# Performance work log

Measured on AMD Instinct MI355X. Metric: run time of the kernel, lower is better.

## Reference

```python
import jax, jax.numpy as jnp
import numpy as np

B, S, E, H = 2, 2048, 1024, 16
D = E // H  # head_dim = 64


def _rope(x):
    # x: (B, H, S, D); torchtune-style interleaved rotary embedding
    s, d = x.shape[-2], x.shape[-1]
    inv_freq = 1.0 / (10000.0 ** (jnp.arange(0, d, 2, dtype=jnp.float32) / d))  # (d/2,)
    freqs = jnp.arange(s, dtype=jnp.float32)[:, None] * inv_freq[None, :]       # (S, d/2)
    cos, sin = jnp.cos(freqs), jnp.sin(freqs)
    x1, x2 = x[..., 0::2], x[..., 1::2]
    o1 = x1 * cos - x2 * sin
    o2 = x2 * cos + x1 * sin
    return jnp.stack([o1, o2], axis=-1).reshape(x.shape)


def setup_inputs() -> dict:
    key = jax.random.key(0)
    kx, kq, kk, kv, ko = jax.random.split(key, 5)
    std = 1.0 / np.sqrt(E)
    return {
        "x": jax.random.normal(kx, (B, S, E), dtype=jnp.float32),
        "W_q": jax.random.normal(kq, (E, E), dtype=jnp.float32) * std,
        "W_k": jax.random.normal(kk, (E, E), dtype=jnp.float32) * std,
        "W_v": jax.random.normal(kv, (E, E), dtype=jnp.float32) * std,
        "W_o": jax.random.normal(ko, (E, E), dtype=jnp.float32) * std,
    }


def reference(x, W_q, W_k, W_v, W_o):
    b, s, e = x.shape
    h, d = H, e // H
    # nn.Linear: y = x @ W.T  (weights are (out, in))
    q = (x @ W_q.T).reshape(b, s, h, d).transpose(0, 2, 1, 3)  # (B,H,S,D)
    k = (x @ W_k.T).reshape(b, s, h, d).transpose(0, 2, 1, 3)
    v = (x @ W_v.T).reshape(b, s, h, d).transpose(0, 2, 1, 3)
    q = _rope(q)
    k = _rope(k)
    attn_scale = 1.0 / np.sqrt(e)  # NOTE: scales by sqrt(hidden_dim), as in source
    scores = jnp.einsum("bhsd,bhtd->bhst", q, k) * attn_scale  # (B,H,S,S)
    causal = jnp.triu(jnp.ones((s, s), dtype=bool), k=1)
    scores = jnp.where(causal, -jnp.inf, scores)
    probs = jax.nn.softmax(scores, axis=-1)  # dropout is identity in eval
    out = jnp.einsum("bhst,bhtd->bhsd", probs, v)
    out = out.transpose(0, 2, 1, 3).reshape(b, s, e)
    return out @ W_o.T
```

## Files before the change

### kernel.cpp

```cpp
#include <hip/hip_runtime.h>
#include <hip/hip_bf16.h>

#define BATCH 2
#define SEQ   2048
#define EMB   1024
#define NH    16
#define HD    64
#define MROWS (BATCH*SEQ)
#define NX    (MROWS*EMB)
#define NW    (EMB*EMB)

using f32x4  = __attribute__((ext_vector_type(4))) float;
using bf16x8 = __attribute__((ext_vector_type(8))) short;

#define GLOBAL_AS(p) ((const __attribute__((address_space(1))) void*)(p))
#define LDS_AS(p)    ((__attribute__((address_space(3))) void*)(p))

#define ROPE_L2 0.4152410118609203f
#define QSCALE  0.045084220027780106f

__global__ void fused_cast_kernel(const float* __restrict__ x,
                                  const float* __restrict__ Wq,
                                  const float* __restrict__ Wk,
                                  const float* __restrict__ Wv,
                                  const float* __restrict__ Wo,
                                  __hip_bfloat16* __restrict__ xb,
                                  __hip_bfloat16* __restrict__ Wqkvb,
                                  __hip_bfloat16* __restrict__ Wob,
                                  float2* __restrict__ ctab) {
    if (blockIdx.x >= 4096) {
        int e  = (blockIdx.x - 4096) * 256 + threadIdx.x;
        int s  = e >> 5;
        int ip = e & 31;
        float inv = exp2f(-(float)ip * ROPE_L2);
        float fr  = (float)s * inv;
        float2 cs;
        cs.x = cosf(fr);
        cs.y = sinf(fr);
        ctab[e] = cs;
        return;
    }
    size_t i8 = (size_t)(blockIdx.x * 256 + threadIdx.x) * 8;
    const float* src;
    __hip_bfloat16* dst;
    if (i8 < (size_t)NX) {
        src = x + i8;
        dst = xb + i8;
    } else {
        size_t w = i8 - NX;
        int which = (int)(w >> 20);
        size_t local = w & (NW - 1);
        if (which < 3) {
            src = (which == 0 ? Wq : (which == 1 ? Wk : Wv)) + local;
            dst = Wqkvb + w;
        } else {
            src = Wo + local;
            dst = Wob + local;
        }
    }
    float4 a = *(const float4*)(src);
    float4 b = *(const float4*)(src + 4);
    union { uint4 u; ushort s[8]; } o;
    const float* f = (const float*)&a;
#pragma unroll
    for (int j = 0; j < 4; ++j) {
        __hip_bfloat16 h = __float2bfloat16(f[j]);
        o.s[j] = *(ushort*)&h;
    }
    f = (const float*)&b;
#pragma unroll
    for (int j = 0; j < 4; ++j) {
        __hip_bfloat16 h = __float2bfloat16(f[j]);
        o.s[4 + j] = *(ushort*)&h;
    }
    *(uint4*)dst = o.u;
}

__global__ __launch_bounds__(256) void gemm_qkv_kernel(
        const __hip_bfloat16* __restrict__ A,
        const __hip_bfloat16* __restrict__ W,
        __hip_bfloat16* __restrict__ Qo,
        __hip_bfloat16* __restrict__ Ko,
        __hip_bfloat16* __restrict__ Vo,
        const float2* __restrict__ ctab, int M, int K) {
    __shared__ __hip_bfloat16 As[128 * 64];
    __shared__ __hip_bfloat16 Bs[128 * 64];

    const int tid  = threadIdx.x;
    const int wave = tid >> 6;
    const int lane = tid & 63;
    const int quad = lane >> 4;
    const int l16  = lane & 15;
    const int m0   = blockIdx.y * 128;
    const int n0   = blockIdx.x * 128;
    const int wm   = (wave >> 1) * 64;
    const int wn   = (wave & 1) * 64;
    const int xr   = l16 & 7;

    f32x4 acc[4][4] = {};

    for (int k0 = 0; k0 < K; k0 += 64) {
#pragma unroll
        for (int it = 0; it < 4; ++it) {
            int flat = (wave * 4 + it) * 64 + lane;
            int row  = flat >> 3;
            int g    = (flat & 7) ^ (row & 7);
            const __hip_bfloat16* ga = A + (size_t)(m0 + row) * K + k0 + g * 8;
            const __hip_bfloat16* gb = W + (size_t)(n0 + row) * K + k0 + g * 8;
            __builtin_amdgcn_global_load_lds(GLOBAL_AS(ga),
                LDS_AS(As + (size_t)(wave * 4 + it) * 512), 16, 0, 0);
            __builtin_amdgcn_global_load_lds(GLOBAL_AS(gb),
                LDS_AS(Bs + (size_t)(wave * 4 + it) * 512), 16, 0, 0);
        }
        __syncthreads();

#pragma unroll
        for (int kk = 0; kk < 2; ++kk) {
            const int kg = (kk * 4 + quad) ^ xr;
            bf16x8 af[4], bfr[4];
#pragma unroll
            for (int i = 0; i < 4; ++i) {
                af[i]  = *(const bf16x8*)(&As[(wm + i * 16 + l16) * 64 + kg * 8]);
                bfr[i] = *(const bf16x8*)(&Bs[(wn + i * 16 + l16) * 64 + kg * 8]);
            }
#pragma unroll
            for (int i = 0; i < 4; ++i)
#pragma unroll
                for (int j = 0; j < 4; ++j)
                    acc[i][j] = __builtin_amdgcn_mfma_f32_16x16x32_bf16(
                        af[i], bfr[j], acc[i][j], 0, 0, 0);
        }
        __syncthreads();
    }

    const int tens = n0 >> 10;
    __hip_bfloat16* outp = (tens == 0) ? Qo : ((tens == 1) ? Ko : Vo);
    const int nbase = n0 & 1023;
    if (tens < 2) {
        const float sgn   = (l16 & 1) ? 1.0f : -1.0f;
        const float qmul  = (tens == 0) ? QSCALE : 1.0f;
#pragma unroll
        for (int i = 0; i < 4; ++i)
#pragma unroll
            for (int j = 0; j < 4; ++j) {
                int col  = nbase + wn + j * 16 + l16;
                int ip   = ((wn + j * 16 + l16) & 63) >> 1;
                int row0 = m0 + wm + i * 16 + quad * 4;
#pragma unroll
                for (int rr = 0; rr < 4; ++rr) {
                    float v = acc[i][j][rr];
                    float p = __shfl_xor(v, 1);
                    int sp  = (row0 + rr) & (SEQ - 1);
                    float2 cs = ctab[sp * 32 + ip];
                    float o = (v * cs.x + sgn * p * cs.y) * qmul;
                    outp[(size_t)(row0 + rr) * EMB + col] = __float2bfloat16(o);
                }
            }
    } else {
#pragma unroll
        for (int i = 0; i < 4; ++i)
#pragma unroll
            for (int j = 0; j < 4; ++j) {
                int col  = nbase + wn + j * 16 + l16;
                int row0 = m0 + wm + i * 16 + quad * 4;
#pragma unroll
                for (int rr = 0; rr < 4; ++rr)
                    outp[(size_t)(row0 + rr) * EMB + col] = __float2bfloat16(acc[i][j][rr]);
            }
    }
}

__global__ __launch_bounds__(256) void gemm_oproj_kernel(
        const __hip_bfloat16* __restrict__ A,
        const __hip_bfloat16* __restrict__ Bm,
        float* __restrict__ C, int M, int N, int K) {
    __shared__ __hip_bfloat16 As[128 * 64];
    __shared__ __hip_bfloat16 Bs[64 * 64];

    const int tid  = threadIdx.x;
    const int wave = tid >> 6;
    const int lane = tid & 63;
    const int quad = lane >> 4;
    const int l16  = lane & 15;
    const int m0   = blockIdx.y * 128;
    const int n0   = blockIdx.x * 64;
    const int wm   = (wave >> 1) * 64;
    const int wn   = (wave & 1) * 32;
    const int xr   = l16 & 7;

    f32x4 acc[4][2] = {};

    for (int k0 = 0; k0 < K; k0 += 64) {
#pragma unroll
        for (int it = 0; it < 4; ++it) {
            int flat = (wave * 4 + it) * 64 + lane;
            int row  = flat >> 3;
            int g    = (flat & 7) ^ (row & 7);
            const __hip_bfloat16* ga = A + (size_t)(m0 + row) * K + k0 + g * 8;
            __builtin_amdgcn_global_load_lds(GLOBAL_AS(ga),
                LDS_AS(As + (size_t)(wave * 4 + it) * 512), 16, 0, 0);
        }
#pragma unroll
        for (int it = 0; it < 2; ++it) {
            int flat = (wave * 2 + it) * 64 + lane;
            int row  = flat >> 3;
            int g    = (flat & 7) ^ (row & 7);
            const __hip_bfloat16* gb = Bm + (size_t)(n0 + row) * K + k0 + g * 8;
            __builtin_amdgcn_global_load_lds(GLOBAL_AS(gb),
                LDS_AS(Bs + (size_t)(wave * 2 + it) * 512), 16, 0, 0);
        }
        __syncthreads();

#pragma unroll
        for (int kk = 0; kk < 2; ++kk) {
            const int kg = (kk * 4 + quad) ^ xr;
            bf16x8 af[4], bfr[2];
#pragma unroll
            for (int i = 0; i < 4; ++i)
                af[i] = *(const bf16x8*)(&As[(wm + i * 16 + l16) * 64 + kg * 8]);
#pragma unroll
            for (int j = 0; j < 2; ++j)
                bfr[j] = *(const bf16x8*)(&Bs[(wn + j * 16 + l16) * 64 + kg * 8]);
#pragma unroll
            for (int i = 0; i < 4; ++i)
#pragma unroll
                for (int j = 0; j < 2; ++j)
                    acc[i][j] = __builtin_amdgcn_mfma_f32_16x16x32_bf16(
                        af[i], bfr[j], acc[i][j], 0, 0, 0);
        }
        __syncthreads();
    }

#pragma unroll
    for (int i = 0; i < 4; ++i)
#pragma unroll
        for (int j = 0; j < 2; ++j) {
            int col  = n0 + wn + j * 16 + l16;
            int row0 = m0 + wm + i * 16 + quad * 4;
#pragma unroll
            for (int rr = 0; rr < 4; ++rr)
                C[(size_t)(row0 + rr) * N + col] = acc[i][j][rr];
        }
}

__device__ inline uint cvt_pk_bf16(float lo, float hi) {
    uint r;
    asm("v_cvt_pk_bf16_f32 %0, %1, %2" : "=v"(r) : "v"(lo), "v"(hi));
    return r;
}
__device__ inline float exp2_raw(float x) {
    float r;
    asm("v_exp_f32 %0, %1" : "=v"(r) : "v"(x));
    return r;
}

__global__ __launch_bounds__(256) void attn_mfma_kernel(
        const __hip_bfloat16* __restrict__ Qb,
        const __hip_bfloat16* __restrict__ Kb,
        const __hip_bfloat16* __restrict__ Vb,
        __hip_bfloat16* __restrict__ Attnb,
        __hip_bfloat16* __restrict__ Opart,
        float* __restrict__ Lpart) {
    const int bx   = blockIdx.x;
    const int bh   = blockIdx.y;
    const int b    = bh >> 4;
    const int h    = bh & (NH - 1);
    const int tid  = threadIdx.x;
    const int wave = tid >> 6;
    const int lane = tid & 63;
    const int quad = lane >> 4;
    const int l16  = lane & 15;

    __shared__ __hip_bfloat16 Ks[2][64 * 64];
    __shared__ uint VTs[2][64][33];

    const int vtp = tid >> 3;
    const int sg  = tid & 7;
    const int lr  = lane >> 3;
    const int lg  = (lane & 7) ^ lr;
    const size_t ksrc_lane = (size_t)lr * EMB + lg * 8;

    const __hip_bfloat16* Kbase = Kb + (size_t)b * SEQ * EMB + h * HD;
    const __hip_bfloat16* Vbase = Vb + (size_t)b * SEQ * EMB + h * HD;

    union { uint u[4]; bf16x8 v; } onesu;
    onesu.u[0] = 0x3F803F80u; onesu.u[1] = 0x3F803F80u;
    onesu.u[2] = 0x3F803F80u; onesu.u[3] = 0x3F803F80u;
    const bf16x8 ones = onesu.v;

    const bool isA = (bx < 16);
    const int p   = isA ? bx : bx - 16;
    const int q0  = 31 - p;
    const int k00 = isA ? 0 : 17;
    const int n0s = isA ? 17 : (15 - p);
    const int q1  = p;
    const int n1s = isA ? 0 : (p + 1);

    for (int s = 0; s < 2; ++s) {
        const int qt = s ? q1 : q0;
        const int k0 = s ? 0 : k00;
        const int nt = s ? n1s : n0s;
        if (nt <= 0) continue;
        const bool finalSeg = (!isA && s == 1);
        const int wrow = qt * 64 + wave * 16;

        __syncthreads();

        bf16x8 qf[2];
        {
            const __hip_bfloat16* qp =
                Qb + (size_t)(b * SEQ + wrow + l16) * EMB + h * HD + quad * 8;
            qf[0] = *(const bf16x8*)(qp);
            qf[1] = *(const bf16x8*)(qp + 32);
        }

        f32x4 of[4]  = {};
        f32x4 of_sum = {};

        const __hip_bfloat16* kgp = Kbase + (size_t)k0 * 64 * EMB;
        const __hip_bfloat16* vgp = Vbase + (size_t)(k0 * 64 + 2 * vtp) * EMB + sg * 8;
        uint4 vr0 = *(const uint4*)(vgp);
        uint4 vr1 = *(const uint4*)(vgp + EMB);
#pragma unroll
        for (int it = 0; it < 2; ++it)
            __builtin_amdgcn_global_load_lds(
                GLOBAL_AS(kgp + (size_t)(wave * 2 + it) * 8 * EMB + ksrc_lane),
                LDS_AS(&Ks[0][(wave * 2 + it) * 512]), 16, 0, 0);

        for (int i = 0; i < nt; ++i) {
            const int cur = i & 1;
            const int kt  = k0 + i;

            {
                const uint* v0u = (const uint*)&vr0;
                const uint* v1u = (const uint*)&vr1;
#pragma unroll
                for (int j = 0; j < 4; ++j) {
                    VTs[cur][sg * 8 + 2 * j][vtp] =
                        __builtin_amdgcn_perm(v1u[j], v0u[j], 0x05040100u);
                    VTs[cur][sg * 8 + 2 * j + 1][vtp] =
                        __builtin_amdgcn_perm(v1u[j], v0u[j], 0x07060302u);
                }
            }
            __syncthreads();

            if (i + 1 < nt) {
                kgp += (size_t)64 * EMB;
                vgp += (size_t)64 * EMB;
                vr0 = *(const uint4*)(vgp);
                vr1 = *(const uint4*)(vgp + EMB);
#pragma unroll
                for (int it = 0; it < 2; ++it)
                    __builtin_amdgcn_global_load_lds(
                        GLOBAL_AS(kgp + (size_t)(wave * 2 + it) * 8 * EMB + ksrc_lane),
                        LDS_AS(&Ks[cur ^ 1][(wave * 2 + it) * 512]), 16, 0, 0);
            }

            const bool diag = (kt == qt);
            const __hip_bfloat16* KsC = Ks[cur];
            f32x4 sc[4];
            __builtin_amdgcn_s_setprio(1);
#pragma unroll
            for (int mb = 0; mb < 4; ++mb) {
                f32x4 a = {};
                if (!(diag && mb > wave)) {
                    int krow = mb * 16 + l16;
#pragma unroll
                    for (int kb = 0; kb < 2; ++kb) {
                        int kg = (kb * 4 + quad) ^ (krow & 7);
                        bf16x8 kf = *(const bf16x8*)(&KsC[krow * 64 + kg * 8]);
                        a = __builtin_amdgcn_mfma_f32_16x16x32_bf16(kf, qf[kb], a, 0, 0, 0);
                    }
                }
                sc[mb] = a;
            }
            __builtin_amdgcn_s_setprio(0);

            if (diag) {
#pragma unroll
                for (int mb = 0; mb < 4; ++mb)
#pragma unroll
                    for (int r = 0; r < 4; ++r)
                        if (mb * 16 + quad * 4 + r > wave * 16 + l16)
                            sc[mb][r] = -16384.0f;
            }

#pragma unroll
            for (int mb = 0; mb < 4; ++mb)
#pragma unroll
                for (int r = 0; r < 4; ++r)
                    sc[mb][r] = exp2_raw(sc[mb][r]);

            bf16x8 pf[2];
            {
                union { uint u[4]; bf16x8 v; } t;
                t.u[0] = cvt_pk_bf16(sc[0][0], sc[0][1]);
                t.u[1] = cvt_pk_bf16(sc[0][2], sc[0][3]);
                t.u[2] = cvt_pk_bf16(sc[1][0], sc[1][1]);
                t.u[3] = cvt_pk_bf16(sc[1][2], sc[1][3]);
                pf[0] = t.v;
                t.u[0] = cvt_pk_bf16(sc[2][0], sc[2][1]);
                t.u[1] = cvt_pk_bf16(sc[2][2], sc[2][3]);
                t.u[2] = cvt_pk_bf16(sc[3][0], sc[3][1]);
                t.u[3] = cvt_pk_bf16(sc[3][2], sc[3][3]);
                pf[1] = t.v;
            }

            const uint* VT0 = &VTs[cur][0][0];
            __builtin_amdgcn_s_setprio(1);
#pragma unroll
            for (int nb = 0; nb < 4; ++nb) {
                const uint* vrow = VT0 + (size_t)(nb * 16 + l16) * 33;
#pragma unroll
                for (int c = 0; c < 2; ++c) {
                    union { uint u[4]; bf16x8 v; } vf;
                    vf.u[0] = vrow[c * 16 + 2 * quad];
                    vf.u[1] = vrow[c * 16 + 2 * quad + 1];
                    vf.u[2] = vrow[c * 16 + 8 + 2 * quad];
                    vf.u[3] = vrow[c * 16 + 8 + 2 * quad + 1];
                    of[nb] = __builtin_amdgcn_mfma_f32_16x16x32_bf16(
                        pf[c], vf.v, of[nb], 0, 0, 0);
                }
            }
            of_sum = __builtin_amdgcn_mfma_f32_16x16x32_bf16(pf[0], ones, of_sum, 0, 0, 0);
            of_sum = __builtin_amdgcn_mfma_f32_16x16x32_bf16(pf[1], ones, of_sum, 0, 0, 0);
            __builtin_amdgcn_s_setprio(0);
        }

        const int rl0 = quad * 4;
        if (finalSeg) {
            float linv[4];
#pragma unroll
            for (int r = 0; r < 4; ++r)
                linv[r] = 1.0f / of_sum[r];
#pragma unroll
            for (int nb = 0; nb < 4; ++nb)
#pragma unroll
                for (int r = 0; r < 4; ++r) {
                    float v = of[nb][r] * linv[r];
                    Attnb[(size_t)(b * SEQ + wrow + rl0 + r) * EMB + h * HD + nb * 16 + l16] =
                        __float2bfloat16(v);
                }
        } else {
            const int slot = isA ? 0 : 1;
            const size_t lbase = ((size_t)slot * 32 + bh) * SEQ + wrow;
            if (l16 == 0) {
#pragma unroll
                for (int r = 0; r < 4; ++r)
                    Lpart[lbase + rl0 + r] = of_sum[r];
            }
#pragma unroll
            for (int nb = 0; nb < 4; ++nb)
#pragma unroll
                for (int r = 0; r < 4; ++r)
                    Opart[(lbase + rl0 + r) * HD + nb * 16 + l16] =
                        __float2bfloat16(of[nb][r]);
        }
    }
}

__global__ void combine_kernel(const __hip_bfloat16* __restrict__ Opart,
                               const float* __restrict__ Lpart,
                               __hip_bfloat16* __restrict__ Attnb) {
    int idx = blockIdx.x * 256 + threadIdx.x;
    int d8 = idx & 7;
    int s  = 1024 + ((idx >> 3) & 1023);
    int bh = idx >> 13;
    int b  = bh >> 4;
    int h  = bh & (NH - 1);
    int qt = s >> 6;

    size_t base0 = ((size_t)bh * SEQ + s) * HD + d8 * 8;
    bf16x8 o0 = *(const bf16x8*)(Opart + base0);
    float l = Lpart[(size_t)bh * SEQ + s];
    float acc[8];
#pragma unroll
    for (int j = 0; j < 8; ++j)
        acc[j] = __uint_as_float(((uint)(ushort)o0[j]) << 16);
    if (qt >= 17) {
        size_t base1 = ((size_t)(32 + bh) * SEQ + s) * HD + d8 * 8;
        bf16x8 o1 = *(const bf16x8*)(Opart + base1);
        l += Lpart[(size_t)(32 + bh) * SEQ + s];
#pragma unroll
        for (int j = 0; j < 8; ++j)
            acc[j] += __uint_as_float(((uint)(ushort)o1[j]) << 16);
    }
    float inv = 1.0f / l;
    union { uint4 u; ushort w[8]; } o;
#pragma unroll
    for (int j = 0; j < 8; ++j) {
        __hip_bfloat16 hv = __float2bfloat16(acc[j] * inv);
        o.w[j] = *(ushort*)&hv;
    }
    *(uint4*)(Attnb + ((size_t)(b * SEQ + s) * EMB) + h * HD + d8 * 8) = o.u;
}

extern "C" void kernel_launch(void* const* d_in, const int* in_sizes, int n_in,
                              void* d_out, int out_size, void* d_ws, size_t ws_size,
                              hipStream_t stream) {
    const float* x  = (const float*)d_in[0];
    const float* Wq = (const float*)d_in[1];
    const float* Wk = (const float*)d_in[2];
    const float* Wv = (const float*)d_in[3];
    const float* Wo = (const float*)d_in[4];
    float* out = (float*)d_out;

    char* ws = (char*)d_ws;
    size_t off = 0;
    auto alloc = [&](size_t bytes) -> void* {
        void* p = ws + off;
        off += (bytes + 255) & ~(size_t)255;
        return p;
    };

    __hip_bfloat16* xb    = (__hip_bfloat16*)alloc((size_t)NX * 2);
    __hip_bfloat16* Wqkvb = (__hip_bfloat16*)alloc((size_t)NW * 3 * 2);
    __hip_bfloat16* Wob   = (__hip_bfloat16*)alloc((size_t)NW * 2);
    __hip_bfloat16* Qbuf  = (__hip_bfloat16*)alloc((size_t)NX * 2);
    __hip_bfloat16* Kbuf  = (__hip_bfloat16*)alloc((size_t)NX * 2);
    __hip_bfloat16* Vbuf  = (__hip_bfloat16*)alloc((size_t)NX * 2);
    __hip_bfloat16* Attnb = (__hip_bfloat16*)alloc((size_t)NX * 2);
    __hip_bfloat16* Opart = (__hip_bfloat16*)alloc((size_t)2 * 32 * SEQ * HD * 2);
    float*          Lpart = (float*)alloc((size_t)2 * 32 * SEQ * 4);
    float2*         ctab  = (float2*)alloc((size_t)SEQ * 32 * sizeof(float2));

    fused_cast_kernel<<<(NX + 4 * NW) / (256 * 8) + 256, 256, 0, stream>>>(
        x, Wq, Wk, Wv, Wo, xb, Wqkvb, Wob, ctab);

    dim3 qgrid(24, MROWS / 128);
    gemm_qkv_kernel<<<qgrid, 256, 0, stream>>>(xb, Wqkvb, Qbuf, Kbuf, Vbuf,
                                               ctab, MROWS, EMB);

    dim3 agrid(32, BATCH * NH);
    attn_mfma_kernel<<<agrid, 256, 0, stream>>>(Qbuf, Kbuf, Vbuf, Attnb,
                                                Opart, Lpart);

    combine_kernel<<<(32 * 1024 * 8) / 256, 256, 0, stream>>>(Opart, Lpart, Attnb);

    dim3 ggrid(EMB / 64, MROWS / 128);
    gemm_oproj_kernel<<<ggrid, 256, 0, stream>>>(Attnb, Wob, out, MROWS, EMB, EMB);
}
```

Baseline: 185.1 us.

## Replace split-KV attention with 128-row query tiles and drop combine kernel

The attention kernel now uses 512-thread blocks that each own a 128-row query tile and walk all causal key tiles, ordered largest-first. This replaces the previous paired split-KV scheme, which wrote partial outputs and sums to workspace and then merged them in a separate combine kernel. Removing that kernel saves one launch and the partial-result memory traffic, and each K/V tile loaded to LDS is now shared by eight waves instead of four. In exchange the grid has 512 blocks of unequal length and no KV splitting, so load balance depends on the longest-first order. Waves of the lower half also sit idle on the last diagonal tile.

Measured after the change: 193.1 us. 4.3% more time.

```diff
diff --git a/kernel.cpp b/kernel.cpp
--- a/kernel.cpp
+++ b/kernel.cpp
@@ -254,15 +254,14 @@
     return r;
 }
 
-__global__ __launch_bounds__(256) void attn_mfma_kernel(
+__global__ __launch_bounds__(512) void attn_mfma_kernel(
         const __hip_bfloat16* __restrict__ Qb,
         const __hip_bfloat16* __restrict__ Kb,
         const __hip_bfloat16* __restrict__ Vb,
-        __hip_bfloat16* __restrict__ Attnb,
-        __hip_bfloat16* __restrict__ Opart,
-        float* __restrict__ Lpart) {
-    const int bx   = blockIdx.x;
-    const int bh   = blockIdx.y;
+        __hip_bfloat16* __restrict__ Attnb) {
+    const int di   = blockIdx.y * 16 + blockIdx.x;
+    const int qt   = 15 - (di >> 5);
+    const int bh   = di & 31;
     const int b    = bh >> 4;
     const int h    = bh & (NH - 1);
     const int tid  = threadIdx.x;
@@ -274,10 +273,11 @@
     __shared__ __hip_bfloat16 Ks[2][64 * 64];
     __shared__ uint VTs[2][64][33];
 
-    const int vtp = tid >> 3;
-    const int sg  = tid & 7;
-    const int lr  = lane >> 3;
-    const int lg  = (lane & 7) ^ lr;
+    const int pc   = tid >> 4;
+    const int sgg  = tid & 15;
+    const int d0   = sgg * 4;
+    const int lr   = lane >> 3;
+    const int lg   = (lane & 7) ^ lr;
     const size_t ksrc_lane = (size_t)lr * EMB + lg * 8;
 
     const __hip_bfloat16* Kbase = Kb + (size_t)b * SEQ * EMB + h * HD;
@@ -288,211 +288,145 @@
     onesu.u[2] = 0x3F803F80u; onesu.u[3] = 0x3F803F80u;
     const bf16x8 ones = onesu.v;
 
-    const bool isA = (bx < 16);
-    const int p   = isA ? bx : bx - 16;
-    const int q0  = 31 - p;
-    const int k00 = isA ? 0 : 17;
-    const int n0s = isA ? 17 : (15 - p);
-    const int q1  = p;
-    const int n1s = isA ? 0 : (p + 1);
-
-    for (int s = 0; s < 2; ++s) {
-        const int qt = s ? q1 : q0;
-        const int k0 = s ? 0 : k00;
-        const int nt = s ? n1s : n0s;
-        if (nt <= 0) continue;
-        const bool finalSeg = (!isA && s == 1);
-        const int wrow = qt * 64 + wave * 16;
-
+    const int  nt      = 2 * qt + 2;
+    const bool lowHalf = (wave < 4);
+    const int  we      = lowHalf ? wave : wave - 4;
+
+    const int qrow0 = qt * 128 + wave * 16;
+    bf16x8 qf[2];
+    {
+        const __hip_bfloat16* qp =
+            Qb + (size_t)(b * SEQ + qrow0 + l16) * EMB + h * HD + quad * 8;
+        qf[0] = *(const bf16x8*)(qp);
+        qf[1] = *(const bf16x8*)(qp + 32);
+    }
+
+    f32x4 of[4]  = {};
+    f32x4 of_sum = {};
+
+    const __hip_bfloat16* kgp = Kbase;
+    const __hip_bfloat16* vgp = Vbase + (size_t)(2 * pc) * EMB + d0;
+    uint2 va = *(const uint2*)(vgp);
+    uint2 vb = *(const uint2*)(vgp + EMB);
+    __builtin_amdgcn_global_load_lds(
+        GLOBAL_AS(kgp + (size_t)(8 * wave) * EMB + ksrc_lane),
+        LDS_AS(&Ks[0][wave * 512]), 16, 0, 0);
+
+    for (int i = 0; i < nt; ++i) {
+        const int cur = i & 1;
+
+        {
+            const uint* vau = (const uint*)&va;
+            const uint* vbu = (const uint*)&vb;
+#pragma unroll
+            for (int j = 0; j < 2; ++j) {
+                VTs[cur][d0 + 2 * j][pc] =
+                    __builtin_amdgcn_perm(vbu[j], vau[j], 0x05040100u);
+                VTs[cur][d0 + 2 * j + 1][pc] =
+                    __builtin_amdgcn_perm(vbu[j], vau[j], 0x07060302u);
+            }
+        }
         __syncthreads();
 
-        bf16x8 qf[2];
+        if (i + 1 < nt) {
+            kgp += (size_t)64 * EMB;
+            vgp += (size_t)64 * EMB;
+            va = *(const uint2*)(vgp);
+            vb = *(const uint2*)(vgp + EMB);
+            __builtin_amdgcn_global_load_lds(
+                GLOBAL_AS(kgp + (size_t)(8 * wave) * EMB + ksrc_lane),
+                LDS_AS(&Ks[cur ^ 1][wave * 512]), 16, 0, 0);
+        }
+
+        const bool diagA = (i == 2 * qt);
+        const bool diagB = (i == 2 * qt + 1);
+        const bool skip  = diagB && lowHalf;
+        if (skip) continue;
+        const bool masking = (diagA && lowHalf) || (diagB && !lowHalf);
+
+        const __hip_bfloat16* KsC = Ks[cur];
+        f32x4 sc[4];
+        __builtin_amdgcn_s_setprio(1);
+#pragma unroll
+        for (int mb = 0; mb < 4; ++mb) {
+            f32x4 a = {};
+            if (!(masking && mb > we)) {
+                int krow = mb * 16 + l16;
+#pragma unroll
+                for (int kb = 0; kb < 2; ++kb) {
+                    int kg = (kb * 4 + quad) ^ (krow & 7);
+                    bf16x8 kf = *(const bf16x8*)(&KsC[krow * 64 + kg * 8]);
+                    a = __builtin_amdgcn_mfma_f32_16x16x32_bf16(kf, qf[kb], a, 0, 0, 0);
+                }
+            }
+            sc[mb] = a;
+        }
+        __builtin_amdgcn_s_setprio(0);
+
+        if (masking) {
+#pragma unroll
+            for (int mb = 0; mb < 4; ++mb)
+#pragma unroll
+                for (int r = 0; r < 4; ++r)
+                    if (mb * 16 + quad * 4 + r > we * 16 + l16)
+                        sc[mb][r] = -16384.0f;
+        }
+
+#pragma unroll
+        for (int mb = 0; mb < 4; ++mb)
+#pragma unroll
+            for (int r = 0; r < 4; ++r)
+                sc[mb][r] = exp2_raw(sc[mb][r]);
+
+        bf16x8 pf[2];
         {
-            const __hip_bfloat16* qp =
-                Qb + (size_t)(b * SEQ + wrow + l16) * EMB + h * HD + quad * 8;
-            qf[0] = *(const bf16x8*)(qp);
-            qf[1] = *(const bf16x8*)(qp + 32);
-        }
-
-        f32x4 of[4]  = {};
-        f32x4 of_sum = {};
-
-        const __hip_bfloat16* kgp = Kbase + (size_t)k0 * 64 * EMB;
-        const __hip_bfloat16* vgp = Vbase + (size_t)(k0 * 64 + 2 * vtp) * EMB + sg * 8;
-        uint4 vr0 = *(const uint4*)(vgp);
-        uint4 vr1 = *(const uint4*)(vgp + EMB);
-#pragma unroll
-        for (int it = 0; it < 2; ++it)
-            __builtin_amdgcn_global_load_lds(
-                GLOBAL_AS(kgp + (size_t)(wave * 2 + it) * 8 * EMB + ksrc_lane),
-                LDS_AS(&Ks[0][(wave * 2 + it) * 512]), 16, 0, 0);
-
-        for (int i = 0; i < nt; ++i) {
-            const int cur = i & 1;
-            const int kt  = k0 + i;
-
-            {
-                const uint* v0u = (const uint*)&vr0;
-                const uint* v1u = (const uint*)&vr1;
-#pragma unroll
-                for (int j = 0; j < 4; ++j) {
-                    VTs[cur][sg * 8 + 2 * j][vtp] =
-                        __builtin_amdgcn_perm(v1u[j], v0u[j], 0x05040100u);
-                    VTs[cur][sg * 8 + 2 * j + 1][vtp] =
-                        __builtin_amdgcn_perm(v1u[j], v0u[j], 0x07060302u);
-                }
-            }
-            __syncthreads();
-
-            if (i + 1 < nt) {
-                kgp += (size_t)64 * EMB;
-                vgp += (size_t)64 * EMB;
-                vr0 = *(const uint4*)(vgp);
-                vr1 = *(const uint4*)(vgp + EMB);
-#pragma unroll
-                for (int it = 0; it < 2; ++it)
-                    __builtin_amdgcn_global_load_lds(
-                        GLOBAL_AS(kgp + (size_t)(wave * 2 + it) * 8 * EMB + ksrc_lane),
-                        LDS_AS(&Ks[cur ^ 1][(wave * 2 + it) * 512]), 16, 0, 0);
-            }
-
-            const bool diag = (kt == qt);
-            const __hip_bfloat16* KsC = Ks[cur];
-            f32x4 sc[4];
-            __builtin_amdgcn_s_setprio(1);
-#pragma unroll
-            for (int mb = 0; mb < 4; ++mb) {
-                f32x4 a = {};
-                if (!(diag && mb > wave)) {
-                    int krow = mb * 16 + l16;
-#pragma unroll
-                    for (int kb = 0; kb < 2; ++kb) {
-                        int kg = (kb * 4 + quad) ^ (krow & 7);
-                        bf16x8 kf = *(const bf16x8*)(&KsC[krow * 64 + kg * 8]);
-                        a = __builtin_amdgcn_mfma_f32_16x16x32_bf16(kf, qf[kb], a, 0, 0, 0);
-                    }
-                }
-                sc[mb] = a;
-            }
-            __builtin_amdgcn_s_setprio(0);
-
-            if (diag) {
-#pragma unroll
-                for (int mb = 0; mb < 4; ++mb)
-#pragma unroll
-                    for (int r = 0; r < 4; ++r)
-                        if (mb * 16 + quad * 4 + r > wave * 16 + l16)
-                            sc[mb][r] = -16384.0f;
-            }
-
-#pragma unroll
-            for (int mb = 0; mb < 4; ++mb)
-#pragma unroll
-                for (int r = 0; r < 4; ++r)
-                    sc[mb][r] = exp2_raw(sc[mb][r]);
-
-            bf16x8 pf[2];
-            {
-                union { uint u[4]; bf16x8 v; } t;
-                t.u[0] = cvt_pk_bf16(sc[0][0], sc[0][1]);
-                t.u[1] = cvt_pk_bf16(sc[0][2], sc[0][3]);
-                t.u[2] = cvt_pk_bf16(sc[1][0], sc[1][1]);
-                t.u[3] = cvt_pk_bf16(sc[1][2], sc[1][3]);
-                pf[0] = t.v;
-                t.u[0] = cvt_pk_bf16(sc[2][0], sc[2][1]);
-                t.u[1] = cvt_pk_bf16(sc[2][2], sc[2][3]);
-                t.u[2] = cvt_pk_bf16(sc[3][0], sc[3][1]);
-                t.u[3] = cvt_pk_bf16(sc[3][2], sc[3][3]);
-                pf[1] = t.v;
-            }
-
-            const uint* VT0 = &VTs[cur][0][0];
-            __builtin_amdgcn_s_setprio(1);
-#pragma unroll
-            for (int nb = 0; nb < 4; ++nb) {
-                const uint* vrow = VT0 + (size_t)(nb * 16 + l16) * 33;
-#pragma unroll
-                for (int c = 0; c < 2; ++c) {
-                    union { uint u[4]; bf16x8 v; } vf;
-                    vf.u[0] = vrow[c * 16 + 2 * quad];
-                    vf.u[1] = vrow[c * 16 + 2 * quad + 1];
-                    vf.u[2] = vrow[c * 16 + 8 + 2 * quad];
-                    vf.u[3] = vrow[c * 16 + 8 + 2 * quad + 1];
-                    of[nb] = __builtin_amdgcn_mfma_f32_16x16x32_bf16(
-                        pf[c], vf.v, of[nb], 0, 0, 0);
-                }
-            }
-            of_sum = __builtin_amdgcn_mfma_f32_16x16x32_bf16(pf[0], ones, of_sum, 0, 0, 0);
-            of_sum = __builtin_amdgcn_mfma_f32_16x16x32_bf16(pf[1], ones, of_sum, 0, 0, 0);
-            __builtin_amdgcn_s_setprio(0);
-        }
-
-        const int rl0 = quad * 4;
-        if (finalSeg) {
-            float linv[4];
-#pragma unroll
-            for (int r = 0; r < 4; ++r)
-                linv[r] = 1.0f / of_sum[r];
-#pragma unroll
-            for (int nb = 0; nb < 4; ++nb)
-#pragma unroll
-                for (int r = 0; r < 4; ++r) {
-                    float v = of[nb][r] * linv[r];
-                    Attnb[(size_t)(b * SEQ + wrow + rl0 + r) * EMB + h * HD + nb * 16 + l16] =
-                        __float2bfloat16(v);
-                }
-        } else {
-            const int slot = isA ? 0 : 1;
-            const size_t lbase = ((size_t)slot * 32 + bh) * SEQ + wrow;
-            if (l16 == 0) {
-#pragma unroll
-                for (int r = 0; r < 4; ++r)
-                    Lpart[lbase + rl0 + r] = of_sum[r];
-            }
-#pragma unroll
-            for (int nb = 0; nb < 4; ++nb)
-#pragma unroll
-                for (int r = 0; r < 4; ++r)
-                    Opart[(lbase + rl0 + r) * HD + nb * 16 + l16] =
-                        __float2bfloat16(of[nb][r]);
-        }
-    }
-}
-
-__global__ void combine_kernel(const __hip_bfloat16* __restrict__ Opart,
-                               const float* __restrict__ Lpart,
-                               __hip_bfloat16* __restrict__ Attnb) {
-    int idx = blockIdx.x * 256 + threadIdx.x;
-    int d8 = idx & 7;
-    int s  = 1024 + ((idx >> 3) & 1023);
-    int bh = idx >> 13;
-    int b  = bh >> 4;
-    int h  = bh & (NH - 1);
-    int qt = s >> 6;
-
-    size_t base0 = ((size_t)bh * SEQ + s) * HD + d8 * 8;
-    bf16x8 o0 = *(const bf16x8*)(Opart + base0);
-    float l = Lpart[(size_t)bh * SEQ + s];
-    float acc[8];
-#pragma unroll
-    for (int j = 0; j < 8; ++j)
-        acc[j] = __uint_as_float(((uint)(ushort)o0[j]) << 16);
-    if (qt >= 17) {
-        size_t base1 = ((size_t)(32 + bh) * SEQ + s) * HD + d8 * 8;
-        bf16x8 o1 = *(const bf16x8*)(Opart + base1);
-        l += Lpart[(size_t)(32 + bh) * SEQ + s];
-#pragma unroll
-        for (int j = 0; j < 8; ++j)
-            acc[j] += __uint_as_float(((uint)(ushort)o1[j]) << 16);
-    }
-    float inv = 1.0f / l;
-    union { uint4 u; ushort w[8]; } o;
-#pragma unroll
-    for (int j = 0; j < 8; ++j) {
-        __hip_bfloat16 hv = __float2bfloat16(acc[j] * inv);
-        o.w[j] = *(ushort*)&hv;
-    }
-    *(uint4*)(Attnb + ((size_t)(b * SEQ + s) * EMB) + h * HD + d8 * 8) = o.u;
+            union { uint u[4]; bf16x8 v; } t;
+            t.u[0] = cvt_pk_bf16(sc[0][0], sc[0][1]);
+            t.u[1] = cvt_pk_bf16(sc[0][2], sc[0][3]);
+            t.u[2] = cvt_pk_bf16(sc[1][0], sc[1][1]);
+            t.u[3] = cvt_pk_bf16(sc[1][2], sc[1][3]);
+            pf[0] = t.v;
+            t.u[0] = cvt_pk_bf16(sc[2][0], sc[2][1]);
+            t.u[1] = cvt_pk_bf16(sc[2][2], sc[2][3]);
+            t.u[2] = cvt_pk_bf16(sc[3][0], sc[3][1]);
+            t.u[3] = cvt_pk_bf16(sc[3][2], sc[3][3]);
+            pf[1] = t.v;
+        }
+
+        const uint* VT0 = &VTs[cur][0][0];
+        __builtin_amdgcn_s_setprio(1);
+#pragma unroll
+        for (int nb = 0; nb < 4; ++nb) {
+            const uint* vrow = VT0 + (size_t)(nb * 16 + l16) * 33;
+#pragma unroll
+            for (int c = 0; c < 2; ++c) {
+                union { uint u[4]; bf16x8 v; } vf;
+                vf.u[0] = vrow[c * 16 + 2 * quad];
+                vf.u[1] = vrow[c * 16 + 2 * quad + 1];
+                vf.u[2] = vrow[c * 16 + 8 + 2 * quad];
+                vf.u[3] = vrow[c * 16 + 8 + 2 * quad + 1];
+                of[nb] = __builtin_amdgcn_mfma_f32_16x16x32_bf16(
+                    pf[c], vf.v, of[nb], 0, 0, 0);
+            }
+        }
+        of_sum = __builtin_amdgcn_mfma_f32_16x16x32_bf16(pf[0], ones, of_sum, 0, 0, 0);
+        of_sum = __builtin_amdgcn_mfma_f32_16x16x32_bf16(pf[1], ones, of_sum, 0, 0, 0);
+        __builtin_amdgcn_s_setprio(0);
+    }
+
+    const int rl0 = quad * 4;
+    float linv[4];
+#pragma unroll
+    for (int r = 0; r < 4; ++r)
+        linv[r] = 1.0f / of_sum[r];
+#pragma unroll
+    for (int nb = 0; nb < 4; ++nb)
+#pragma unroll
+        for (int r = 0; r < 4; ++r) {
+            float v = of[nb][r] * linv[r];
+            Attnb[(size_t)(b * SEQ + qrow0 + rl0 + r) * EMB + h * HD + nb * 16 + l16] =
+                __float2bfloat16(v);
+        }
 }
 
 extern "C" void kernel_launch(void* const* d_in, const int* in_sizes, int n_in,
@@ -520,8 +454,6 @@
     __hip_bfloat16* Kbuf  = (__hip_bfloat16*)alloc((size_t)NX * 2);
     __hip_bfloat16* Vbuf  = (__hip_bfloat16*)alloc((size_t)NX * 2);
     __hip_bfloat16* Attnb = (__hip_bfloat16*)alloc((size_t)NX * 2);
-    __hip_bfloat16* Opart = (__hip_bfloat16*)alloc((size_t)2 * 32 * SEQ * HD * 2);
-    float*          Lpart = (float*)alloc((size_t)2 * 32 * SEQ * 4);
     float2*         ctab  = (float2*)alloc((size_t)SEQ * 32 * sizeof(float2));
 
     fused_cast_kernel<<<(NX + 4 * NW) / (256 * 8) + 256, 256, 0, stream>>>(
@@ -531,11 +463,8 @@
     gemm_qkv_kernel<<<qgrid, 256, 0, stream>>>(xb, Wqkvb, Qbuf, Kbuf, Vbuf,
                                                ctab, MROWS, EMB);
 
-    dim3 agrid(32, BATCH * NH);
-    attn_mfma_kernel<<<agrid, 256, 0, stream>>>(Qbuf, Kbuf, Vbuf, Attnb,
-                                                Opart, Lpart);
-
-    combine_kernel<<<(32 * 1024 * 8) / 256, 256, 0, stream>>>(Opart, Lpart, Attnb);
+    dim3 agrid(16, 32);
+    attn_mfma_kernel<<<agrid, 512, 0, stream>>>(Qbuf, Kbuf, Vbuf, Attnb);
 
     dim3 ggrid(EMB / 64, MROWS / 128);
     gemm_oproj_kernel<<<ggrid, 256, 0, stream>>>(Attnb, Wob, out, MROWS, EMB, EMB);
```
